# Performance work log

Measured on AMD Instinct MI355X. Metric: run time of the kernel, lower is better.

Reference implementation:

```python
import jax, jax.numpy as jnp
import numpy as np

S, B, D, HID, OUT = 96, 16, 512, 128, 2


def setup_inputs() -> dict:
    key = jax.random.key(0)
    ks = jax.random.split(key, 6)
    embeds = jax.random.normal(ks[0], (S, B, D), dtype=jnp.float32)
    embeds_cmp = jax.random.normal(ks[1], (S, B, D), dtype=jnp.float32)
    umask = jnp.ones((B, S), dtype=jnp.float32)   # unused by the math
    qmask = jnp.zeros((S, B, 2), dtype=jnp.float32)  # unused by the math
    # fc: Linear(2*D -> HID); classify: Linear(HID -> OUT)
    W1 = jax.random.normal(ks[2], (HID, 2 * D), dtype=jnp.float32) * 0.02
    b1 = jnp.zeros((HID,), dtype=jnp.float32)
    W2 = jax.random.normal(ks[3], (OUT, HID), dtype=jnp.float32) * 0.02
    b2 = jnp.zeros((OUT,), dtype=jnp.float32)
    return {"embeds": embeds, "umask": umask, "qmask": qmask,
            "embeds_cmp": embeds_cmp, "W1": W1, "b1": b1, "W2": W2, "b2": b2}


def reference(embeds, umask, qmask, embeds_cmp, W1, b1, W2, b2):
    # Pairwise concat [embeds_i ; embeds_cmp_j] -> Linear(2D->HID).
    # Split W1 into halves so the quadratic concat is never materialized:
    # concat(x1,x2) @ W1^T == x1 @ W1a^T + x2 @ W1b^T (same math, fused form).
    d = embeds.shape[-1]
    W1a, W1b = W1[:, :d], W1[:, d:]
    ha = jnp.einsum('ibd,hd->ibh', embeds, W1a)        # [S,B,HID]
    hb = jnp.einsum('jbd,hd->jbh', embeds_cmp, W1b)    # [S,B,HID]
    h = jax.nn.relu(ha[:, None] + hb[None, :] + b1)    # [S,S,B,HID]
    # Dropout(p=0.9) is identity in eval mode.
    logits = jnp.einsum('ijbh,ch->ijbc', h, W2) + b2   # [S,S,B,2]
    return logits
```

## Files before the change

### kernel.cpp

```cpp
#include <hip/hip_runtime.h>

#define S_   96
#define B_   16
#define D_   512
#define HID_ 128
#define M_   (S_ * B_)
#define KC_  4
#define KCH_ (D_ / KC_)
#define CHF_ (2 * M_ * HID_)

typedef __attribute__((ext_vector_type(4))) float        f32x4_t;
typedef __attribute__((ext_vector_type(2))) float        f32x2_t;
typedef __attribute__((ext_vector_type(4))) unsigned int u32x4_t;
typedef __attribute__((ext_vector_type(8))) short        short8;

static __device__ __forceinline__ void split8(f32x4_t a, f32x4_t b,
                                              short8& hi, short8& lo) {
    float f[8];
    #pragma unroll
    for (int j = 0; j < 4; ++j) { f[j] = a[j]; f[4 + j] = b[j]; }
    unsigned int hb[8], lb[8];
    #pragma unroll
    for (int j = 0; j < 8; ++j) {
        unsigned int u = __float_as_uint(f[j]);
        float hf = __uint_as_float(u & 0xffff0000u);
        hb[j] = u >> 16;
        lb[j] = __float_as_uint(f[j] - hf) >> 16;
    }
    union { u32x4_t u; short8 s; } H, L;
    #pragma unroll
    for (int j = 0; j < 4; ++j) {
        H.u[j] = hb[2 * j] | (hb[2 * j + 1] << 16);
        L.u[j] = lb[2 * j] | (lb[2 * j + 1] << 16);
    }
    hi = H.s; lo = L.s;
}

__global__ __launch_bounds__(256) void stage1_mfma(
    const float* __restrict__ emb,
    const float* __restrict__ embc,
    const float* __restrict__ W1,
    const float* __restrict__ b1,
    float* __restrict__ ws)
{
    const int wave = threadIdx.x >> 6;
    const int lane = threadIdx.x & 63;
    const int gm = blockIdx.x * 64 + wave * 16;
    const int z  = (gm >= M_) ? 1 : 0;
    const int m0 = gm - z * M_;
    const int n0 = blockIdx.y * 16;
    const int kc = blockIdx.z;

    const int rsel = lane & 15;
    const int kq   = (lane >> 4) * 8;
    const float* xr = (z ? embc : emb) + (m0 + rsel) * D_ + kc * KCH_ + kq;
    const float* wr = W1 + (n0 + rsel) * (2 * D_) + z * D_ + kc * KCH_ + kq;

    f32x4_t acc = {0.f, 0.f, 0.f, 0.f};
    #pragma unroll
    for (int k = 0; k < KCH_; k += 32) {
        f32x4_t xa = *(const f32x4_t*)(xr + k);
        f32x4_t xb = *(const f32x4_t*)(xr + k + 4);
        f32x4_t wa = *(const f32x4_t*)(wr + k);
        f32x4_t wb = *(const f32x4_t*)(wr + k + 4);
        short8 xhi, xlo, whi, wlo;
        split8(xa, xb, xhi, xlo);
        split8(wa, wb, whi, wlo);
        acc = __builtin_amdgcn_mfma_f32_16x16x32_bf16(xhi, whi, acc, 0, 0, 0);
        acc = __builtin_amdgcn_mfma_f32_16x16x32_bf16(xhi, wlo, acc, 0, 0, 0);
        acc = __builtin_amdgcn_mfma_f32_16x16x32_bf16(xlo, whi, acc, 0, 0, 0);
    }

    const int h = n0 + rsel;
    const float bias = (z == 0 && kc == 0) ? b1[h] : 0.f;
    const int mrow = m0 + (lane >> 4) * 4;
    float* dst = ws + (size_t)kc * CHF_ + (size_t)z * (M_ * HID_);
    #pragma unroll
    for (int r = 0; r < 4; ++r) {
        dst[(mrow + r) * HID_ + h] = acc[r] + bias;
    }
}

__global__ __launch_bounds__(256) void stage2(
    const float* __restrict__ ws,
    const float* __restrict__ W2,
    const float* __restrict__ b2,
    float* __restrict__ out)
{
    __shared__ float ha_s[16 * 132];
    __shared__ float hb_s[16 * 132];
    __shared__ float w2_s[2 * HID_];

    const int t  = threadIdx.x;
    const int i0 = blockIdx.x * 16;
    const int j0 = blockIdx.y * 16;
    const int b  = blockIdx.z;

    {
        const int r = t >> 4;
        const int c = (t & 15) * 8;
        const float* pHa = ws + ((i0 + r) * B_ + b) * HID_ + c;
        const float* pHb = ws + (M_ * HID_) + ((j0 + r) * B_ + b) * HID_ + c;
        f32x4_t a0 = *(const f32x4_t*)pHa,       a1 = *(const f32x4_t*)(pHa + 4);
        f32x4_t b0 = *(const f32x4_t*)pHb,       b1v = *(const f32x4_t*)(pHb + 4);
        #pragma unroll
        for (int kc = 1; kc < KC_; ++kc) {
            const float* qa = pHa + (size_t)kc * CHF_;
            const float* qb = pHb + (size_t)kc * CHF_;
            a0  += *(const f32x4_t*)qa;       a1  += *(const f32x4_t*)(qa + 4);
            b0  += *(const f32x4_t*)qb;       b1v += *(const f32x4_t*)(qb + 4);
        }
        *(f32x4_t*)&ha_s[r * 132 + c]     = a0;
        *(f32x4_t*)&ha_s[r * 132 + c + 4] = a1;
        *(f32x4_t*)&hb_s[r * 132 + c]     = b0;
        *(f32x4_t*)&hb_s[r * 132 + c + 4] = b1v;
        w2_s[t] = W2[t];
    }
    __syncthreads();

    const int ti = t >> 4, tj = t & 15;
    const float* pa = &ha_s[ti * 132];
    const float* pb = &hb_s[tj * 132];
    float acc0 = 0.f, acc1 = 0.f;
    #pragma unroll
    for (int h = 0; h < HID_; h += 4) {
        f32x4_t av = *(const f32x4_t*)(pa + h);
        f32x4_t bv = *(const f32x4_t*)(pb + h);
        f32x4_t w0 = *(const f32x4_t*)&w2_s[h];
        f32x4_t w1 = *(const f32x4_t*)&w2_s[HID_ + h];
        #pragma unroll
        for (int q = 0; q < 4; ++q) {
            float v = fmaxf(av[q] + bv[q], 0.f);
            acc0 = fmaf(v, w0[q], acc0);
            acc1 = fmaf(v, w1[q], acc1);
        }
    }

    const int i = i0 + ti, j = j0 + tj;
    const int idx = ((i * S_ + j) * B_ + b) * 2;
    f32x2_t o = { acc0 + b2[0], acc1 + b2[1] };
    *(f32x2_t*)(out + idx) = o;
}

__global__ __launch_bounds__(256) void fused_fallback(
    const float* __restrict__ emb,
    const float* __restrict__ embc,
    const float* __restrict__ W1,
    const float* __restrict__ b1,
    const float* __restrict__ W2,
    const float* __restrict__ b2,
    float* __restrict__ out)
{
    __shared__ float ha_s[16 * 132];
    __shared__ float hb_s[16 * 132];
    __shared__ float w2_s[2 * HID_];

    const int t  = threadIdx.x;
    const int i0 = blockIdx.x * 16;
    const int j0 = blockIdx.y * 16;
    const int b  = blockIdx.z;

    w2_s[t] = W2[t];

    for (int o = t; o < 4096; o += 256) {
        const int side = o >> 11;
        const int mi   = (o >> 7) & 15;
        const int h    = o & 127;
        const int srow = ((side ? j0 : i0) + mi) * B_ + b;
        const float* x = (side ? embc : emb) + srow * D_;
        const float* w = W1 + h * (2 * D_) + side * D_;
        float s = side ? 0.f : b1[h];
        for (int d = 0; d < D_; d += 4) {
            f32x4_t xv = *(const f32x4_t*)(x + d);
            f32x4_t wv = *(const f32x4_t*)(w + d);
            s = fmaf(xv[0], wv[0], s);
            s = fmaf(xv[1], wv[1], s);
            s = fmaf(xv[2], wv[2], s);
            s = fmaf(xv[3], wv[3], s);
        }
        (side ? hb_s : ha_s)[mi * 132 + h] = s;
    }
    __syncthreads();

    const int ti = t >> 4, tj = t & 15;
    const float* pa = &ha_s[ti * 132];
    const float* pb = &hb_s[tj * 132];
    float acc0 = 0.f, acc1 = 0.f;
    #pragma unroll
    for (int h = 0; h < HID_; h += 4) {
        f32x4_t av = *(const f32x4_t*)(pa + h);
        f32x4_t bv = *(const f32x4_t*)(pb + h);
        f32x4_t w0 = *(const f32x4_t*)&w2_s[h];
        f32x4_t w1 = *(const f32x4_t*)&w2_s[HID_ + h];
        #pragma unroll
        for (int q = 0; q < 4; ++q) {
            float v = fmaxf(av[q] + bv[q], 0.f);
            acc0 = fmaf(v, w0[q], acc0);
            acc1 = fmaf(v, w1[q], acc1);
        }
    }
    const int i = i0 + ti, j = j0 + tj;
    const int idx = ((i * S_ + j) * B_ + b) * 2;
    f32x2_t ov = { acc0 + b2[0], acc1 + b2[1] };
    *(f32x2_t*)(out + idx) = ov;
}

extern "C" void kernel_launch(void* const* d_in, const int* in_sizes, int n_in,
                              void* d_out, int out_size, void* d_ws, size_t ws_size,
                              hipStream_t stream) {
    const float* emb  = (const float*)d_in[0];
    const float* embc = (const float*)d_in[3];
    const float* W1   = (const float*)d_in[4];
    const float* b1   = (const float*)d_in[5];
    const float* W2   = (const float*)d_in[6];
    const float* b2   = (const float*)d_in[7];
    float* out = (float*)d_out;

    const size_t need = (size_t)KC_ * CHF_ * sizeof(float);
    if (d_ws != nullptr && ws_size >= need) {
        float* ws = (float*)d_ws;
        stage1_mfma<<<dim3(48, 8, KC_), 256, 0, stream>>>(emb, embc, W1, b1, ws);
        stage2<<<dim3(6, 6, 16), 256, 0, stream>>>(ws, W2, b2, out);
    } else {
        fused_fallback<<<dim3(6, 6, 16), 256, 0, stream>>>(emb, embc, W1, b1, W2, b2, out);
    }
}
```

Baseline: 94.76 us.

## Tile stage1 GEMM through LDS with 64x64 block tiles and 2x2 MFMA per wave

Stage1 now stages a 64-row by 128-wide chunk of the embeddings and a 64-row chunk of W1 into shared memory, and each wave computes a 32x32 sub-tile with a 2x2 grid of MFMAs. The old version had every wave reload its operands straight from global memory for a single 16x16 output tile. The goal is to reuse each loaded operand across several MFMAs and cut redundant global traffic. The cost is 4x fewer blocks (grid y goes from 8 to 2), about 67KB of LDS per block which limits occupancy, and bf16 splitting of the same shared-memory data done again in each wave.

```diff
diff --git a/kernel.cpp b/kernel.cpp
--- a/kernel.cpp
+++ b/kernel.cpp
@@ -43,41 +43,75 @@
     const float* __restrict__ b1,
     float* __restrict__ ws)
 {
-    const int wave = threadIdx.x >> 6;
-    const int lane = threadIdx.x & 63;
-    const int gm = blockIdx.x * 64 + wave * 16;
-    const int z  = (gm >= M_) ? 1 : 0;
-    const int m0 = gm - z * M_;
-    const int n0 = blockIdx.y * 16;
-    const int kc = blockIdx.z;
+    __shared__ float x_s[64 * 132];
+    __shared__ float w_s[64 * 132];
+
+    const int t    = threadIdx.x;
+    const int wave = t >> 6;
+    const int lane = t & 63;
+    const int bx   = blockIdx.x;
+    const int h0   = blockIdx.y * 64;
+    const int kc   = blockIdx.z;
+
+    const int z    = (bx >= 24) ? 1 : 0;
+    const int mloc = bx * 64 - z * M_;
+
+    const float* xbase = (z ? embc : emb) + (size_t)mloc * D_ + kc * KCH_;
+    const float* wbase = W1 + (size_t)h0 * (2 * D_) + z * D_ + kc * KCH_;
+
+    #pragma unroll
+    for (int rep = 0; rep < 8; ++rep) {
+        const int idx = rep * 256 + t;
+        const int row = idx >> 5;
+        const int c4  = (idx & 31) * 4;
+        *(f32x4_t*)&x_s[row * 132 + c4] = *(const f32x4_t*)(xbase + row * D_ + c4);
+        *(f32x4_t*)&w_s[row * 132 + c4] = *(const f32x4_t*)(wbase + row * (2 * D_) + c4);
+    }
+    __syncthreads();
 
     const int rsel = lane & 15;
     const int kq   = (lane >> 4) * 8;
-    const float* xr = (z ? embc : emb) + (m0 + rsel) * D_ + kc * KCH_ + kq;
-    const float* wr = W1 + (n0 + rsel) * (2 * D_) + z * D_ + kc * KCH_ + kq;
-
-    f32x4_t acc = {0.f, 0.f, 0.f, 0.f};
-    #pragma unroll
-    for (int k = 0; k < KCH_; k += 32) {
-        f32x4_t xa = *(const f32x4_t*)(xr + k);
-        f32x4_t xb = *(const f32x4_t*)(xr + k + 4);
-        f32x4_t wa = *(const f32x4_t*)(wr + k);
-        f32x4_t wb = *(const f32x4_t*)(wr + k + 4);
-        short8 xhi, xlo, whi, wlo;
-        split8(xa, xb, xhi, xlo);
-        split8(wa, wb, whi, wlo);
-        acc = __builtin_amdgcn_mfma_f32_16x16x32_bf16(xhi, whi, acc, 0, 0, 0);
-        acc = __builtin_amdgcn_mfma_f32_16x16x32_bf16(xhi, wlo, acc, 0, 0, 0);
-        acc = __builtin_amdgcn_mfma_f32_16x16x32_bf16(xlo, whi, acc, 0, 0, 0);
-    }
-
-    const int h = n0 + rsel;
-    const float bias = (z == 0 && kc == 0) ? b1[h] : 0.f;
-    const int mrow = m0 + (lane >> 4) * 4;
+    const int wm   = (wave & 1) * 32;
+    const int wh   = (wave >> 1) * 32;
+
+    f32x4_t acc[2][2] = {{{0.f,0.f,0.f,0.f},{0.f,0.f,0.f,0.f}},
+                         {{0.f,0.f,0.f,0.f},{0.f,0.f,0.f,0.f}}};
+    #pragma unroll
+    for (int kk = 0; kk < KCH_; kk += 32) {
+        short8 ahi[2], alo[2], bhi[2], blo[2];
+        #pragma unroll
+        for (int ms = 0; ms < 2; ++ms) {
+            const float* p = &x_s[(wm + ms * 16 + rsel) * 132 + kk + kq];
+            split8(*(const f32x4_t*)p, *(const f32x4_t*)(p + 4), ahi[ms], alo[ms]);
+        }
+        #pragma unroll
+        for (int hs = 0; hs < 2; ++hs) {
+            const float* p = &w_s[(wh + hs * 16 + rsel) * 132 + kk + kq];
+            split8(*(const f32x4_t*)p, *(const f32x4_t*)(p + 4), bhi[hs], blo[hs]);
+        }
+        #pragma unroll
+        for (int ms = 0; ms < 2; ++ms)
+            #pragma unroll
+            for (int hs = 0; hs < 2; ++hs) {
+                acc[ms][hs] = __builtin_amdgcn_mfma_f32_16x16x32_bf16(ahi[ms], bhi[hs], acc[ms][hs], 0, 0, 0);
+                acc[ms][hs] = __builtin_amdgcn_mfma_f32_16x16x32_bf16(ahi[ms], blo[hs], acc[ms][hs], 0, 0, 0);
+                acc[ms][hs] = __builtin_amdgcn_mfma_f32_16x16x32_bf16(alo[ms], bhi[hs], acc[ms][hs], 0, 0, 0);
+            }
+    }
+
     float* dst = ws + (size_t)kc * CHF_ + (size_t)z * (M_ * HID_);
-    #pragma unroll
-    for (int r = 0; r < 4; ++r) {
-        dst[(mrow + r) * HID_ + h] = acc[r] + bias;
+    const int mrow_base = mloc + wm + (lane >> 4) * 4;
+    #pragma unroll
+    for (int ms = 0; ms < 2; ++ms) {
+        #pragma unroll
+        for (int hs = 0; hs < 2; ++hs) {
+            const int h = h0 + wh + hs * 16 + rsel;
+            const float bias = (z == 0 && kc == 0) ? b1[h] : 0.f;
+            #pragma unroll
+            for (int r = 0; r < 4; ++r) {
+                dst[(mrow_base + ms * 16 + r) * HID_ + h] = acc[ms][hs][r] + bias;
+            }
+        }
     }
 }
 
@@ -101,14 +135,14 @@
         const int c = (t & 15) * 8;
         const float* pHa = ws + ((i0 + r) * B_ + b) * HID_ + c;
         const float* pHb = ws + (M_ * HID_) + ((j0 + r) * B_ + b) * HID_ + c;
-        f32x4_t a0 = *(const f32x4_t*)pHa,       a1 = *(const f32x4_t*)(pHa + 4);
-        f32x4_t b0 = *(const f32x4_t*)pHb,       b1v = *(const f32x4_t*)(pHb + 4);
+        f32x4_t a0 = *(const f32x4_t*)pHa,  a1  = *(const f32x4_t*)(pHa + 4);
+        f32x4_t b0 = *(const f32x4_t*)pHb,  b1v = *(const f32x4_t*)(pHb + 4);
         #pragma unroll
         for (int kc = 1; kc < KC_; ++kc) {
             const float* qa = pHa + (size_t)kc * CHF_;
             const float* qb = pHb + (size_t)kc * CHF_;
-            a0  += *(const f32x4_t*)qa;       a1  += *(const f32x4_t*)(qa + 4);
-            b0  += *(const f32x4_t*)qb;       b1v += *(const f32x4_t*)(qb + 4);
+            a0  += *(const f32x4_t*)qa;   a1  += *(const f32x4_t*)(qa + 4);
+            b0  += *(const f32x4_t*)qb;   b1v += *(const f32x4_t*)(qb + 4);
         }
         *(f32x4_t*)&ha_s[r * 132 + c]     = a0;
         *(f32x4_t*)&ha_s[r * 132 + c + 4] = a1;
@@ -219,7 +253,7 @@
     const size_t need = (size_t)KC_ * CHF_ * sizeof(float);
     if (d_ws != nullptr && ws_size >= need) {
         float* ws = (float*)d_ws;
-        stage1_mfma<<<dim3(48, 8, KC_), 256, 0, stream>>>(emb, embc, W1, b1, ws);
+        stage1_mfma<<<dim3(48, 2, KC_), 256, 0, stream>>>(emb, embc, W1, b1, ws);
         stage2<<<dim3(6, 6, 16), 256, 0, stream>>>(ws, W2, b2, out);
     } else {
         fused_fallback<<<dim3(6, 6, 16), 256, 0, stream>>>(emb, embc, W1, b1, W2, b2, out);
```

Result: faster. 88.21 us (-6.9%).
